# Kernel optimization log

Measured on AMD Instinct MI355X. Metric: run time of the kernel, lower is better.

Reference implementation:

```python
import jax, jax.numpy as jnp
import numpy as np

NUM_TAG = 128
T, B = 1024, 512


def setup_inputs() -> dict:
    key = jax.random.key(0)
    k_em, k_tag, k_s, k_t, k_e = jax.random.split(key, 5)
    emissions = jax.random.normal(k_em, (T, B, NUM_TAG), dtype=jnp.float32)
    tags = jax.random.randint(k_tag, (T, B), 0, NUM_TAG, dtype=jnp.int32)
    mask = jnp.ones((T, B), dtype=jnp.float32)
    # parameters: uniform(-0.1, 0.1) as in reset_params
    start_transitions = jax.random.uniform(k_s, (NUM_TAG,), minval=-0.1, maxval=0.1, dtype=jnp.float32)
    transitions = jax.random.uniform(k_t, (NUM_TAG, NUM_TAG), minval=-0.1, maxval=0.1, dtype=jnp.float32)
    end_transitions = jax.random.uniform(k_e, (NUM_TAG,), minval=-0.1, maxval=0.1, dtype=jnp.float32)
    return {
        "emissions": emissions,
        "tags": tags,
        "mask": mask,
        "start_transitions": start_transitions,
        "transitions": transitions,
        "end_transitions": end_transitions,
    }


def _path_score(emissions, tags, mask, start_transitions, transitions, end_transitions):
    # emissions: [T,B,K], tags/mask: [T,B]
    b_idx = jnp.arange(tags.shape[1])
    # emission score of the gold tag at each step: [T,B]
    em_tag = jnp.take_along_axis(emissions, tags[:, :, None].astype(jnp.int32), axis=2)[:, :, 0]
    scores = start_transitions[tags[0]] + (em_tag * mask).sum(axis=0)
    # transition scores along the gold path, masked: [T-1,B]
    scores = scores + (transitions[tags[:-1], tags[1:]] * mask[1:]).sum(axis=0)
    last_idx = mask.astype(jnp.int32).sum(axis=0) - 1  # [B]
    last_tag = tags[last_idx, b_idx]
    return scores + end_transitions[last_tag]


def _log_partition(emissions, mask, start_transitions, transitions, end_transitions):
    log_prob0 = start_transitions[None, :] + emissions[0]  # [B,K]

    def step(log_prob, xs):
        em_t, m_t = xs  # [B,K], [B]
        # score[b,i,j] = log_prob[b,i] + transitions[i,j] + em_t[b,j]
        score = jax.nn.logsumexp(
            log_prob[:, :, None] + transitions[None, :, :] + em_t[:, None, :], axis=1
        )
        new_lp = score * m_t[:, None] + log_prob * (1.0 - m_t)[:, None]
        return new_lp, None

    log_prob, _ = jax.lax.scan(step, log_prob0, (emissions[1:], mask[1:]))
    return jax.nn.logsumexp(log_prob + end_transitions[None, :], axis=1)  # [B]


def reference(emissions, tags, mask, start_transitions, transitions, end_transitions):
    path = _path_score(emissions, tags, mask, start_transitions, transitions, end_transitions)
    log_z = _log_partition(emissions, mask, start_transitions, transitions, end_transitions)
    return (path - log_z).sum()
```

## Files before the change

### kernel.cpp

```cpp
#include <hip/hip_runtime.h>
#include <cstdint>

#define TT 1024
#define BB 512
#define KK 128

__device__ __forceinline__ float rl(float v, int lane) {
  return __uint_as_float((unsigned)__builtin_amdgcn_readlane(__float_as_uint(v), lane));
}

__global__ __launch_bounds__(256, 2) void crf_forward(
    const float* __restrict__ em, const float* __restrict__ mask,
    const float* __restrict__ start_t, const float* __restrict__ trans,
    const float* __restrict__ end_t, float* __restrict__ logz)
{
  const int b    = blockIdx.x;
  const int tid  = threadIdx.x;
  const int lane = tid & 63;
  const int w    = __builtin_amdgcn_readfirstlane(tid >> 6);
  const int c0   = lane * 2;

  __shared__ float smp[2][4][KK];

  float E0[32], E1[32];
#pragma unroll
  for (int ki = 0; ki < 32; ++ki) {
    const float2 tv = *reinterpret_cast<const float2*>(trans + (size_t)(32 * w + ki) * KK + c0);
    E0[ki] = __expf(tv.x);
    E1[ki] = __expf(tv.y);
  }

  const float* em_b = em + (size_t)b * KK + c0;

  float rel0, rel1, p0, p1, base;
  {
    const float2 st = *reinterpret_cast<const float2*>(start_t + c0);
    const float2 e0 = *reinterpret_cast<const float2*>(em_b);
    float nq0 = st.x + e0.x, nq1 = st.y + e0.y;
    float m = fmaxf(nq0, nq1);
#pragma unroll
    for (int off = 32; off; off >>= 1) m = fmaxf(m, __shfl_xor(m, off));
    base = m;
    rel0 = nq0 - m; rel1 = nq1 - m;
    p0 = __expf(rel0); p1 = __expf(rel1);
  }

  float2 em_n = *reinterpret_cast<const float2*>(em_b + (size_t)1 * BB * KK);
  float  mk_n = mask[1 * BB + b];

  for (int t = 1; t < TT; ++t) {
    const int buf = t & 1;
    const float2 em_c = em_n;
    const float  mk_c = mk_n;
    if (t < TT - 1) {
      em_n = *reinterpret_cast<const float2*>(em_b + (size_t)(t + 1) * BB * KK);
      mk_n = mask[(t + 1) * BB + b];
    }

    float a0 = 0.f, a1 = 0.f;
#pragma unroll
    for (int jj = 0; jj < 16; ++jj) {
      const float q0 = rl(p0, 16 * w + jj);
      const float q1 = rl(p1, 16 * w + jj);
      a0 = fmaf(q0, E0[2 * jj], a0);
      a1 = fmaf(q0, E1[2 * jj], a1);
      a0 = fmaf(q1, E0[2 * jj + 1], a0);
      a1 = fmaf(q1, E1[2 * jj + 1], a1);
    }
    *reinterpret_cast<float2*>(&smp[buf][w][c0]) = make_float2(a0, a1);
    __syncthreads();

    const float2 pa = *reinterpret_cast<const float2*>(&smp[buf][0][c0]);
    const float2 pb = *reinterpret_cast<const float2*>(&smp[buf][1][c0]);
    const float2 pc = *reinterpret_cast<const float2*>(&smp[buf][2][c0]);
    const float2 pd = *reinterpret_cast<const float2*>(&smp[buf][3][c0]);
    const float s0 = (pa.x + pb.x) + (pc.x + pd.x);
    const float s1 = (pa.y + pb.y) + (pc.y + pd.y);

    const bool upd = (mk_c != 0.f);
    const float nq0 = upd ? (__logf(s0) + em_c.x) : rel0;
    const float nq1 = upd ? (__logf(s1) + em_c.y) : rel1;

    float m = fmaxf(nq0, nq1);
#pragma unroll
    for (int off = 32; off; off >>= 1) m = fmaxf(m, __shfl_xor(m, off));
    base += m;
    rel0 = nq0 - m; rel1 = nq1 - m;
    p0 = __expf(rel0); p1 = __expf(rel1);
  }

  {
    const float2 ed = *reinterpret_cast<const float2*>(end_t + c0);
    const float v0 = rel0 + ed.x, v1 = rel1 + ed.y;
    float m = fmaxf(v0, v1);
#pragma unroll
    for (int off = 32; off; off >>= 1) m = fmaxf(m, __shfl_xor(m, off));
    float s = __expf(v0 - m) + __expf(v1 - m);
#pragma unroll
    for (int off = 32; off; off >>= 1) s += __shfl_xor(s, off);
    if (tid == 0) logz[b] = base + m + __logf(s);
  }
}

__global__ __launch_bounds__(256) void crf_path(
    const float* __restrict__ em, const int* __restrict__ tags,
    const float* __restrict__ mask, const float* __restrict__ start_t,
    const float* __restrict__ trans, const float* __restrict__ end_t,
    float* __restrict__ path_out)
{
  const int b = blockIdx.x;
  const int tid = threadIdx.x;
  float acc = 0.f, msum = 0.f;
  for (int t = tid; t < TT; t += 256) {
    const int   tg = tags[t * BB + b];
    const float mk = mask[t * BB + b];
    msum += mk;
    acc = fmaf(em[((size_t)t * BB + b) * KK + tg], mk, acc);
    if (t >= 1) {
      const int tgp = tags[(t - 1) * BB + b];
      acc = fmaf(trans[tgp * KK + tg], mk, acc);
    }
  }
  __shared__ float red_a[4], red_m[4];
#pragma unroll
  for (int off = 32; off; off >>= 1) {
    acc  += __shfl_xor(acc, off);
    msum += __shfl_xor(msum, off);
  }
  if ((tid & 63) == 0) { red_a[tid >> 6] = acc; red_m[tid >> 6] = msum; }
  __syncthreads();
  if (tid == 0) {
    float a  = (red_a[0] + red_a[1]) + (red_a[2] + red_a[3]);
    float ms = (red_m[0] + red_m[1]) + (red_m[2] + red_m[3]);
    const int last = (int)(ms + 0.5f) - 1;
    a += start_t[tags[b]] + end_t[tags[(size_t)last * BB + b]];
    path_out[b] = a;
  }
}

__global__ __launch_bounds__(512) void crf_final(
    const float* __restrict__ path, const float* __restrict__ logz,
    float* __restrict__ out)
{
  const int tid = threadIdx.x;
  float v = path[tid] - logz[tid];
  __shared__ float red[8];
#pragma unroll
  for (int off = 32; off; off >>= 1) v += __shfl_xor(v, off);
  if ((tid & 63) == 0) red[tid >> 6] = v;
  __syncthreads();
  if (tid == 0) {
    float s = 0.f;
#pragma unroll
    for (int i = 0; i < 8; ++i) s += red[i];
    out[0] = s;
  }
}

extern "C" void kernel_launch(void* const* d_in, const int* in_sizes, int n_in,
                              void* d_out, int out_size, void* d_ws, size_t ws_size,
                              hipStream_t stream) {
  const float* em    = (const float*)d_in[0];
  const int*   tags  = (const int*)  d_in[1];
  const float* mask  = (const float*)d_in[2];
  const float* st    = (const float*)d_in[3];
  const float* trans = (const float*)d_in[4];
  const float* et    = (const float*)d_in[5];
  float* out = (float*)d_out;

  float* ws_path = (float*)d_ws;
  float* ws_logz = ws_path + BB;

  crf_path   <<<BB, 256, 0, stream>>>(em, tags, mask, st, trans, et, ws_path);
  crf_forward<<<BB, 256, 0, stream>>>(em, mask, st, trans, et, ws_logz);
  crf_final  <<<1, 512, 0, stream>>>(ws_path, ws_logz, out);
}
```

Before: 1.296 ms.

## Batch 16 sequences per block and compute CRF forward recursion with bf16 MFMA

The forward recursion now processes 16 batch rows per block and does the exp-space matrix product on bf16 MFMA instructions instead of one batch row per block with scalar FMAs and readlane broadcasts. Probabilities are staged in LDS as bf16, and per-row maxima are shared through LDS for lagged normalization. A lightweight waitcnt+barrier replaces __syncthreads. Only 32 blocks are launched, so most CUs sit idle, and bf16 rounding of probabilities and exp(transitions) reduces accuracy.

```diff
diff --git a/kernel.cpp b/kernel.cpp
--- a/kernel.cpp
+++ b/kernel.cpp
@@ -5,100 +5,198 @@
 #define BB 512
 #define KK 128
 
-__device__ __forceinline__ float rl(float v, int lane) {
-  return __uint_as_float((unsigned)__builtin_amdgcn_readlane(__float_as_uint(v), lane));
-}
-
-__global__ __launch_bounds__(256, 2) void crf_forward(
+typedef __attribute__((ext_vector_type(8))) short short8;
+typedef __attribute__((ext_vector_type(4))) float f4;
+
+__device__ __forceinline__ unsigned short f2bf(float x) {
+  unsigned u = __float_as_uint(x);
+  u += 0x7FFF + ((u >> 16) & 1);
+  return (unsigned short)(u >> 16);
+}
+
+__device__ __forceinline__ void lgkm_barrier() {
+  __atomic_signal_fence(__ATOMIC_SEQ_CST);
+  __builtin_amdgcn_s_waitcnt(0xC07F);
+  __builtin_amdgcn_s_barrier();
+  __atomic_signal_fence(__ATOMIC_SEQ_CST);
+}
+
+__global__ __launch_bounds__(256, 1) void crf_forward(
     const float* __restrict__ em, const float* __restrict__ mask,
     const float* __restrict__ start_t, const float* __restrict__ trans,
     const float* __restrict__ end_t, float* __restrict__ logz)
 {
-  const int b    = blockIdx.x;
   const int tid  = threadIdx.x;
+  const int w    = __builtin_amdgcn_readfirstlane(tid >> 6);
   const int lane = tid & 63;
-  const int w    = __builtin_amdgcn_readfirstlane(tid >> 6);
-  const int c0   = lane * 2;
-
-  __shared__ float smp[2][4][KK];
-
-  float E0[32], E1[32];
-#pragma unroll
-  for (int ki = 0; ki < 32; ++ki) {
-    const float2 tv = *reinterpret_cast<const float2*>(trans + (size_t)(32 * w + ki) * KK + c0);
-    E0[ki] = __expf(tv.x);
-    E1[ki] = __expf(tv.y);
-  }
-
-  const float* em_b = em + (size_t)b * KK + c0;
-
-  float rel0, rel1, p0, p1, base;
+  const int q    = lane >> 4;
+  const int lo   = lane & 15;
+  const int b0   = blockIdx.x * 16;
+
+  __shared__ __align__(16) unsigned short Pt[2][16 * 136];
+  __shared__ __align__(16) float mxs[2][16][4];
+  __shared__ __align__(16) float psm[16][4];
+  __shared__ float bs[16];
+
+  const int n0      = w * 32 + lo;
+  const int laneoff = q * 4 * KK + n0;
+
+  const float* em0p = em + (size_t)b0 * KK;
+  const float* em1p = em + ((size_t)BB + b0) * KK;
+  float e0v[4][2], emc[4][2], mkc[4];
+#pragma unroll
+  for (int r = 0; r < 4; ++r) {
+    e0v[r][0] = em0p[laneoff + r * KK];
+    e0v[r][1] = em0p[laneoff + r * KK + 16];
+    emc[r][0] = em1p[laneoff + r * KK];
+    emc[r][1] = em1p[laneoff + r * KK + 16];
+    mkc[r]    = mask[BB + b0 + 4 * q + r];
+  }
+  const float st0 = start_t[n0], st1 = start_t[n0 + 16];
+
+  short8 Bf[2][4];
+#pragma unroll
+  for (int nt = 0; nt < 2; ++nt)
+#pragma unroll
+    for (int kt = 0; kt < 4; ++kt) {
+      short8 v;
+#pragma unroll
+      for (int j = 0; j < 8; ++j) {
+        const int k = kt * 32 + q * 8 + j;
+        v[j] = (short)f2bf(__expf(trans[(size_t)k * KK + n0 + nt * 16]));
+      }
+      Bf[nt][kt] = v;
+    }
+
+  float rel[4][2], base[4];
+#pragma unroll
+  for (int r = 0; r < 4; ++r) {
+    rel[r][0] = st0 + e0v[r][0];
+    rel[r][1] = st1 + e0v[r][1];
+    base[r]   = 0.f;
+  }
+
+#pragma unroll
+  for (int r = 0; r < 4; ++r) {
+    const int m = 4 * q + r;
+    Pt[0][m * 136 + n0]      = f2bf(__expf(rel[r][0]));
+    Pt[0][m * 136 + n0 + 16] = f2bf(__expf(rel[r][1]));
+  }
   {
-    const float2 st = *reinterpret_cast<const float2*>(start_t + c0);
-    const float2 e0 = *reinterpret_cast<const float2*>(em_b);
-    float nq0 = st.x + e0.x, nq1 = st.y + e0.y;
-    float m = fmaxf(nq0, nq1);
-#pragma unroll
-    for (int off = 32; off; off >>= 1) m = fmaxf(m, __shfl_xor(m, off));
-    base = m;
-    rel0 = nq0 - m; rel1 = nq1 - m;
-    p0 = __expf(rel0); p1 = __expf(rel1);
-  }
-
-  float2 em_n = *reinterpret_cast<const float2*>(em_b + (size_t)1 * BB * KK);
-  float  mk_n = mask[1 * BB + b];
-
+    float vm[4];
+#pragma unroll
+    for (int r = 0; r < 4; ++r) vm[r] = fmaxf(rel[r][0], rel[r][1]);
+#pragma unroll
+    for (int off = 1; off < 16; off <<= 1)
+#pragma unroll
+      for (int r = 0; r < 4; ++r) vm[r] = fmaxf(vm[r], __shfl_xor(vm[r], off));
+    if (lo == 0)
+#pragma unroll
+      for (int r = 0; r < 4; ++r) mxs[0][4 * q + r][w] = vm[r];
+  }
+  lgkm_barrier();
+
+  short8 Af[4];
+  float  Mr[4];
+#pragma unroll
+  for (int kt = 0; kt < 4; ++kt)
+    Af[kt] = *(const short8*)&Pt[0][lo * 136 + kt * 32 + q * 8];
+#pragma unroll
+  for (int r = 0; r < 4; ++r) {
+    const f4 mv = *(const f4*)&mxs[0][4 * q + r][0];
+    Mr[r] = fmaxf(fmaxf(mv[0], mv[1]), fmaxf(mv[2], mv[3]));
+  }
+
+  float emn[4][2], mkn[4];
   for (int t = 1; t < TT; ++t) {
     const int buf = t & 1;
-    const float2 em_c = em_n;
-    const float  mk_c = mk_n;
+
     if (t < TT - 1) {
-      em_n = *reinterpret_cast<const float2*>(em_b + (size_t)(t + 1) * BB * KK);
-      mk_n = mask[(t + 1) * BB + b];
-    }
-
-    float a0 = 0.f, a1 = 0.f;
-#pragma unroll
-    for (int jj = 0; jj < 16; ++jj) {
-      const float q0 = rl(p0, 16 * w + jj);
-      const float q1 = rl(p1, 16 * w + jj);
-      a0 = fmaf(q0, E0[2 * jj], a0);
-      a1 = fmaf(q0, E1[2 * jj], a1);
-      a0 = fmaf(q1, E0[2 * jj + 1], a0);
-      a1 = fmaf(q1, E1[2 * jj + 1], a1);
-    }
-    *reinterpret_cast<float2*>(&smp[buf][w][c0]) = make_float2(a0, a1);
+      const float* emt = em + ((size_t)(t + 1) * BB + b0) * KK;
+#pragma unroll
+      for (int r = 0; r < 4; ++r) {
+        emn[r][0] = emt[laneoff + r * KK];
+        emn[r][1] = emt[laneoff + r * KK + 16];
+        mkn[r]    = mask[(t + 1) * BB + b0 + 4 * q + r];
+      }
+    }
+
+    f4 a0 = {0.f, 0.f, 0.f, 0.f}, a1 = {0.f, 0.f, 0.f, 0.f};
+#pragma unroll
+    for (int kt = 0; kt < 4; ++kt) {
+      a0 = __builtin_amdgcn_mfma_f32_16x16x32_bf16(Af[kt], Bf[0][kt], a0, 0, 0, 0);
+      a1 = __builtin_amdgcn_mfma_f32_16x16x32_bf16(Af[kt], Bf[1][kt], a1, 0, 0, 0);
+    }
+
+#pragma unroll
+    for (int r = 0; r < 4; ++r) {
+      const bool upd = (mkc[r] != 0.f);
+      const float l0 = __logf(a0[r]) + emc[r][0] - Mr[r];
+      const float l1 = __logf(a1[r]) + emc[r][1] - Mr[r];
+      rel[r][0] = upd ? l0 : rel[r][0];
+      rel[r][1] = upd ? l1 : rel[r][1];
+      base[r]  += upd ? Mr[r] : 0.f;
+    }
+
+#pragma unroll
+    for (int r = 0; r < 4; ++r) {
+      const int m = 4 * q + r;
+      Pt[buf][m * 136 + n0]      = f2bf(__expf(rel[r][0]));
+      Pt[buf][m * 136 + n0 + 16] = f2bf(__expf(rel[r][1]));
+    }
+    {
+      float vm[4];
+#pragma unroll
+      for (int r = 0; r < 4; ++r) vm[r] = fmaxf(rel[r][0], rel[r][1]);
+#pragma unroll
+      for (int off = 1; off < 16; off <<= 1)
+#pragma unroll
+        for (int r = 0; r < 4; ++r) vm[r] = fmaxf(vm[r], __shfl_xor(vm[r], off));
+      if (lo == 0)
+#pragma unroll
+        for (int r = 0; r < 4; ++r) mxs[buf][4 * q + r][w] = vm[r];
+    }
+
+    lgkm_barrier();
+
+#pragma unroll
+    for (int kt = 0; kt < 4; ++kt)
+      Af[kt] = *(const short8*)&Pt[buf][lo * 136 + kt * 32 + q * 8];
+#pragma unroll
+    for (int r = 0; r < 4; ++r) {
+      const f4 mv = *(const f4*)&mxs[buf][4 * q + r][0];
+      Mr[r] = fmaxf(fmaxf(mv[0], mv[1]), fmaxf(mv[2], mv[3]));
+    }
+
+#pragma unroll
+    for (int r = 0; r < 4; ++r) {
+      emc[r][0] = emn[r][0];
+      emc[r][1] = emn[r][1];
+      mkc[r]    = mkn[r];
+    }
+  }
+
+  {
+    const float e0 = end_t[n0], e1 = end_t[n0 + 16];
+    float ps[4];
+#pragma unroll
+    for (int r = 0; r < 4; ++r)
+      ps[r] = __expf(rel[r][0] + e0 - Mr[r]) + __expf(rel[r][1] + e1 - Mr[r]);
+#pragma unroll
+    for (int off = 1; off < 16; off <<= 1)
+#pragma unroll
+      for (int r = 0; r < 4; ++r) ps[r] += __shfl_xor(ps[r], off);
+    if (lo == 0)
+#pragma unroll
+      for (int r = 0; r < 4; ++r) {
+        psm[4 * q + r][w] = ps[r];
+        if (w == 0) bs[4 * q + r] = base[r] + Mr[r];
+      }
     __syncthreads();
-
-    const float2 pa = *reinterpret_cast<const float2*>(&smp[buf][0][c0]);
-    const float2 pb = *reinterpret_cast<const float2*>(&smp[buf][1][c0]);
-    const float2 pc = *reinterpret_cast<const float2*>(&smp[buf][2][c0]);
-    const float2 pd = *reinterpret_cast<const float2*>(&smp[buf][3][c0]);
-    const float s0 = (pa.x + pb.x) + (pc.x + pd.x);
-    const float s1 = (pa.y + pb.y) + (pc.y + pd.y);
-
-    const bool upd = (mk_c != 0.f);
-    const float nq0 = upd ? (__logf(s0) + em_c.x) : rel0;
-    const float nq1 = upd ? (__logf(s1) + em_c.y) : rel1;
-
-    float m = fmaxf(nq0, nq1);
-#pragma unroll
-    for (int off = 32; off; off >>= 1) m = fmaxf(m, __shfl_xor(m, off));
-    base += m;
-    rel0 = nq0 - m; rel1 = nq1 - m;
-    p0 = __expf(rel0); p1 = __expf(rel1);
-  }
-
-  {
-    const float2 ed = *reinterpret_cast<const float2*>(end_t + c0);
-    const float v0 = rel0 + ed.x, v1 = rel1 + ed.y;
-    float m = fmaxf(v0, v1);
-#pragma unroll
-    for (int off = 32; off; off >>= 1) m = fmaxf(m, __shfl_xor(m, off));
-    float s = __expf(v0 - m) + __expf(v1 - m);
-#pragma unroll
-    for (int off = 32; off; off >>= 1) s += __shfl_xor(s, off);
-    if (tid == 0) logz[b] = base + m + __logf(s);
+    if (tid < 16) {
+      const f4 pv = *(const f4*)&psm[tid][0];
+      logz[b0 + tid] = bs[tid] + __logf(pv[0] + pv[1] + pv[2] + pv[3]);
+    }
   }
 }
 
@@ -160,6 +258,7 @@
 extern "C" void kernel_launch(void* const* d_in, const int* in_sizes, int n_in,
                               void* d_out, int out_size, void* d_ws, size_t ws_size,
                               hipStream_t stream) {
+  (void)in_sizes; (void)n_in; (void)out_size; (void)ws_size;
   const float* em    = (const float*)d_in[0];
   const int*   tags  = (const int*)  d_in[1];
   const float* mask  = (const float*)d_in[2];
@@ -172,6 +271,6 @@
   float* ws_logz = ws_path + BB;
 
   crf_path   <<<BB, 256, 0, stream>>>(em, tags, mask, st, trans, et, ws_path);
-  crf_forward<<<BB, 256, 0, stream>>>(em, mask, st, trans, et, ws_logz);
+  crf_forward<<<32, 256, 0, stream>>>(em, mask, st, trans, et, ws_logz);
   crf_final  <<<1, 512, 0, stream>>>(ws_path, ws_logz, out);
 }
```

Result: slower. 1.392 ms (+7.4%).
